# Optimization experiments

Measured on AMD Instinct MI355X. Metric: run time of the kernel, lower is better.

Reference implementation:

```python
import jax, jax.numpy as jnp
import numpy as np

N = 50000      # B*N nodes
K = 32         # top-k in-degree
E = N * K      # edges
IN_DIM = 128
EMB_DIM = 128
OUT_DIM = 128
HEADS = 4
D_HEAD = OUT_DIM // HEADS


def setup_inputs() -> dict:
    key = jax.random.key(0)
    ks = jax.random.split(key, 8)
    x = jax.random.normal(ks[0], (N, IN_DIM), dtype=jnp.float32)
    emb = jax.random.normal(ks[1], (N, EMB_DIM), dtype=jnp.float32)
    # top-k graph: each node i has exactly K in-neighbors (dst covers all nodes)
    dst = jnp.repeat(jnp.arange(N, dtype=jnp.int32), K)
    src = jax.random.randint(ks[2], (E,), 0, N, dtype=jnp.int32)
    edge_index = jnp.stack([src, dst], axis=0)
    # learned params (stored as (in, out); math-equivalent to torch Linear)
    W_q = jax.random.normal(ks[3], (EMB_DIM, OUT_DIM), dtype=jnp.float32) / np.sqrt(EMB_DIM)
    W_k = jax.random.normal(ks[4], (EMB_DIM, OUT_DIM), dtype=jnp.float32) / np.sqrt(EMB_DIM)
    W_v = jax.random.normal(ks[5], (IN_DIM + EMB_DIM, OUT_DIM), dtype=jnp.float32) / np.sqrt(IN_DIM + EMB_DIM)
    attn_vec = jax.random.normal(ks[6], (HEADS, 2 * D_HEAD), dtype=jnp.float32) / np.sqrt(2 * D_HEAD)
    ln_gamma = jnp.ones((OUT_DIM,), dtype=jnp.float32)
    ln_beta = jnp.zeros((OUT_DIM,), dtype=jnp.float32)
    return {"x": x, "emb": emb, "edge_index": edge_index, "W_q": W_q, "W_k": W_k,
            "W_v": W_v, "attn_vec": attn_vec, "ln_gamma": ln_gamma, "ln_beta": ln_beta}


def reference(x, emb, edge_index, W_q, W_k, W_v, attn_vec, ln_gamma, ln_beta):
    src, dst = edge_index[0], edge_index[1]
    BN = x.shape[0]
    H, D = HEADS, D_HEAD
    Q = (emb @ W_q).reshape(BN, H, D)
    K_ = (emb @ W_k).reshape(BN, H, D)
    # a^T [q_dst || k_src] = (a_q . q)_dst + (a_k . k)_src  (standard GAT split)
    a_q, a_k = attn_vec[:, :D], attn_vec[:, D:]
    sq = jnp.einsum('nhd,hd->nh', Q, a_q)   # (BN, H)
    sk = jnp.einsum('nhd,hd->nh', K_, a_k)  # (BN, H)
    e = sq[dst] + sk[src]                   # (E, H)
    e = jnp.where(e > 0, e, 0.2 * e)        # LeakyReLU(0.2)
    # segment softmax over incoming edges of each dst node
    e_max = jax.ops.segment_max(e, dst, num_segments=BN)
    e_exp = jnp.exp(e - e_max[dst])
    e_sum = jax.ops.segment_sum(e_exp, dst, num_segments=BN)
    alpha = e_exp / (e_sum[dst] + 1e-8)     # (E, H); dropout is identity at eval
    V = (jnp.concatenate([x, emb], axis=-1) @ W_v).reshape(BN, H, D)
    weighted = alpha[..., None] * V[src]    # (E, H, D)
    z = jax.ops.segment_sum(weighted, dst, num_segments=BN).reshape(BN, H * D)
    z = jax.nn.elu(z)
    mu = jnp.mean(z, axis=-1, keepdims=True)
    var = jnp.var(z, axis=-1, keepdims=True)
    return (z - mu) / jnp.sqrt(var + 1e-5) * ln_gamma + ln_beta
```

## Files before the change

kernel.cpp:

```cpp
#include <hip/hip_runtime.h>

#define NN 50000
#define KE 32
#define PAD_N 50048

using f32x4  = __attribute__((ext_vector_type(4))) float;
using bf16x8 = __attribute__((ext_vector_type(8))) short;

__device__ __forceinline__ ushort f2bf(float f) {
    union { float f; unsigned u; } c; c.f = f;
    unsigned u = c.u;
    u += 0x7fffu + ((u >> 16) & 1u);
    return (ushort)(u >> 16);
}

__global__ __launch_bounds__(256) void prep_kernel(const float* __restrict__ Wq,
        const float* __restrict__ Wk, const float* __restrict__ av,
        const float* __restrict__ Wv, ushort* __restrict__ Ub,
        ushort* __restrict__ Bt) {
    const int g = blockIdx.x * 256 + threadIdx.x;
    if (blockIdx.x < 2) {
        const int h = g >> 7, i = g & 127;
        float su = 0.f, sv = 0.f;
#pragma unroll
        for (int d = 0; d < 32; ++d) {
            su += Wq[i * 128 + h * 32 + d] * av[h * 64 + d];
            sv += Wk[i * 128 + h * 32 + d] * av[h * 64 + 32 + d];
        }
        Ub[h * 128 + i] = f2bf(su);
        Ub[(4 + h) * 128 + i] = f2bf(sv);
        Ub[1024 + g * 2] = 0;
        Ub[1024 + g * 2 + 1] = 0;
    } else {
        const int idx = g - 512;
        const int k = idx >> 7, n = idx & 127;
        Bt[n * 256 + k] = f2bf(Wv[idx]);
    }
}

__global__ __launch_bounds__(256) void vproj_mfma(const float* __restrict__ x,
        const float* __restrict__ emb, const ushort* __restrict__ Bt,
        const ushort* __restrict__ Ub, float* __restrict__ sqT,
        float* __restrict__ skT, ushort* __restrict__ Vp) {
    __shared__ short As[64 * 264];
    const int t = threadIdx.x;
    const int rbase = blockIdx.x * 64;
    const int wv = t >> 6;
    const int lane = t & 63;
    const int lo = lane & 15;
    const int quad = lane >> 4;
    const int c0 = wv * 32;

#pragma unroll
    for (int it = 0; it < 16; ++it) {
        const int li = it * 256 + t;
        const int row = li >> 6;
        const int c4 = li & 63;
        int rg = rbase + row; if (rg >= NN) rg = NN - 1;
        const float* sp = (c4 < 32) ? (x + (long)rg * 128 + c4 * 4)
                                    : (emb + (long)rg * 128 + (c4 - 32) * 4);
        float4 a = *(const float4*)sp;
        ushort4 b = make_ushort4(f2bf(a.x), f2bf(a.y), f2bf(a.z), f2bf(a.w));
        *(ushort4*)&As[row * 264 + c4 * 4] = b;
    }
    bf16x8 bt0[8], bt1[8];
#pragma unroll
    for (int ks = 0; ks < 8; ++ks) {
        const int kb = ks * 32 + quad * 8;
        bt0[ks] = *(const bf16x8*)(Bt + (c0 + lo) * 256 + kb);
        bt1[ks] = *(const bf16x8*)(Bt + (c0 + 16 + lo) * 256 + kb);
    }
    __syncthreads();

    f32x4 acc[4][2] = {};
#pragma unroll
    for (int ks = 0; ks < 8; ++ks) {
        const int kb = ks * 32 + quad * 8;
#pragma unroll
        for (int rt = 0; rt < 4; ++rt) {
            bf16x8 af = *(const bf16x8*)&As[(rt * 16 + lo) * 264 + kb];
            acc[rt][0] = __builtin_amdgcn_mfma_f32_16x16x32_bf16(af, bt0[ks], acc[rt][0], 0, 0, 0);
            acc[rt][1] = __builtin_amdgcn_mfma_f32_16x16x32_bf16(af, bt1[ks], acc[rt][1], 0, 0, 0);
        }
    }

    f32x4 sacc = {};
#pragma unroll
    for (int ks = 0; ks < 4; ++ks) {
        const int kk = ks * 32 + quad * 8;
        bf16x8 saf = *(const bf16x8*)&As[(wv * 16 + lo) * 264 + 128 + kk];
        bf16x8 sbf = *(const bf16x8*)(Ub + lo * 128 + kk);
        sacc = __builtin_amdgcn_mfma_f32_16x16x32_bf16(saf, sbf, sacc, 0, 0, 0);
    }
    if (lo < 8) {
#pragma unroll
        for (int r = 0; r < 4; ++r) {
            const int row = rbase + wv * 16 + quad * 4 + r;
            if (row < NN) {
                if (lo < 4) sqT[(long)lo * NN + row] = sacc[r];
                else        skT[(long)(lo - 4) * NN + row] = sacc[r];
            }
        }
    }

    __syncthreads();
#pragma unroll
    for (int rt = 0; rt < 4; ++rt)
#pragma unroll
        for (int ct = 0; ct < 2; ++ct)
#pragma unroll
            for (int r = 0; r < 4; ++r)
                As[(rt * 16 + quad * 4 + r) * 132 + c0 + ct * 16 + lo] =
                    (short)f2bf(acc[rt][ct][r]);
    __syncthreads();
#pragma unroll
    for (int i = 0; i < 4; ++i) {
        const int idx = i * 256 + t;
        const int row = idx >> 4;
        const int seg = idx & 15;
        const int grow = rbase + row;
        const int plane = seg >> 2;
        const int pc = (seg & 3) * 8;
        if (grow < NN)
            *(bf16x8*)(Vp + (long)plane * PAD_N * 32 + (long)grow * 32 + pc) =
                *(const bf16x8*)&As[row * 132 + seg * 8];
    }
}

__global__ __launch_bounds__(256) void gather_kernel(const int* __restrict__ src,
        const float* __restrict__ sqT, const float* __restrict__ skT,
        const ushort* __restrict__ Vp, float* __restrict__ z) {
    __shared__ int   s_src[64 * 33];
    __shared__ float s_al [64 * 33];
    const int b = blockIdx.x;
    const int head = (b & 7) >> 1;
    const int chunk = (b >> 3) * 2 + (b & 1);
    const int nbase = chunk * 64;
    const int t = threadIdx.x;
    const int e = t & 31;

    const float* sqh = sqT + (long)head * NN;
    const float* skh = skT + (long)head * NN;
#pragma unroll
    for (int p = 0; p < 8; ++p) {
        const int slot = p * 8 + (t >> 5);
        const int n = nbase + slot;
        const bool valid = n < NN;
        const int s = valid ? src[(long)n * KE + e] : 0;
        float ev = valid ? (sqh[n] + skh[s]) : 0.f;
        ev = ev > 0.f ? ev : 0.2f * ev;
        float m = ev;
#pragma unroll
        for (int off = 16; off > 0; off >>= 1)
            m = fmaxf(m, __shfl_xor(m, off));
        const float ex = __expf(ev - m);
        float sum = ex;
#pragma unroll
        for (int off = 16; off > 0; off >>= 1)
            sum += __shfl_xor(sum, off);
        s_src[slot * 33 + e] = s;
        s_al[slot * 33 + e] = ex / (sum + 1e-8f);
    }
    __syncthreads();

    const int slot = t >> 2;
    const int l = t & 3;
    const ushort* plane = Vp + (long)head * PAD_N * 32 + l * 8;
    float z0 = 0.f, z1 = 0.f, z2 = 0.f, z3 = 0.f;
    float z4 = 0.f, z5 = 0.f, z6 = 0.f, z7 = 0.f;
#pragma unroll 16
    for (int ee = 0; ee < 32; ++ee) {
        const int sidx = s_src[slot * 33 + ee];
        const float a = s_al[slot * 33 + ee];
        uint4 p = *(const uint4*)(plane + (long)sidx * 32);
        union { unsigned u; float f; } c0e, c0o, c1e, c1o, c2e, c2o, c3e, c3o;
        c0e.u = p.x << 16; c0o.u = p.x & 0xffff0000u;
        c1e.u = p.y << 16; c1o.u = p.y & 0xffff0000u;
        c2e.u = p.z << 16; c2o.u = p.z & 0xffff0000u;
        c3e.u = p.w << 16; c3o.u = p.w & 0xffff0000u;
        z0 += a * c0e.f; z1 += a * c0o.f;
        z2 += a * c1e.f; z3 += a * c1o.f;
        z4 += a * c2e.f; z5 += a * c2o.f;
        z6 += a * c3e.f; z7 += a * c3o.f;
    }
    const int node = nbase + slot;
    if (node < NN) {
        float* zp = z + (long)node * 128 + head * 32 + l * 8;
        *(float4*)(zp)     = make_float4(z0, z1, z2, z3);
        *(float4*)(zp + 4) = make_float4(z4, z5, z6, z7);
    }
}

__global__ __launch_bounds__(256) void lnorm_kernel(float* __restrict__ z,
        const float* __restrict__ gamma, const float* __restrict__ beta) {
    const int w = threadIdx.x >> 6;
    const int lane = threadIdx.x & 63;
    const int n = blockIdx.x * 4 + w;
    const int c0 = lane * 2;
    float2 zv = *(const float2*)(z + (long)n * 128 + c0);
    float zx = zv.x, zy = zv.y;
    zx = zx > 0.f ? zx : __expf(zx) - 1.f;
    zy = zy > 0.f ? zy : __expf(zy) - 1.f;
    float s1 = zx + zy;
    float s2 = zx * zx + zy * zy;
#pragma unroll
    for (int off = 32; off > 0; off >>= 1) {
        s1 += __shfl_xor(s1, off);
        s2 += __shfl_xor(s2, off);
    }
    const float mu = s1 * (1.f / 128.f);
    const float var = s2 * (1.f / 128.f) - mu * mu;
    const float rstd = rsqrtf(var + 1e-5f);
    float2 g = *(const float2*)(gamma + c0);
    float2 b = *(const float2*)(beta + c0);
    float2 o;
    o.x = (zx - mu) * rstd * g.x + b.x;
    o.y = (zy - mu) * rstd * g.y + b.y;
    *(float2*)(z + (long)n * 128 + c0) = o;
}

extern "C" void kernel_launch(void* const* d_in, const int* in_sizes, int n_in,
                              void* d_out, int out_size, void* d_ws, size_t ws_size,
                              hipStream_t stream) {
    const float* x     = (const float*)d_in[0];
    const float* emb   = (const float*)d_in[1];
    const int*   edge  = (const int*)d_in[2];
    const float* Wq    = (const float*)d_in[3];
    const float* Wk    = (const float*)d_in[4];
    const float* Wv    = (const float*)d_in[5];
    const float* av    = (const float*)d_in[6];
    const float* gamma = (const float*)d_in[7];
    const float* beta  = (const float*)d_in[8];
    float* out = (float*)d_out;

    char* ws = (char*)d_ws;
    ushort* Ub  = (ushort*)(ws + 0);
    ushort* Bt  = (ushort*)(ws + 4096);
    float*  sqT = (float*)(ws + 69632);
    float*  skT = (float*)(ws + 869632);
    ushort* Vp  = (ushort*)(ws + 1669632);

    prep_kernel<<<130, 256, 0, stream>>>(Wq, Wk, av, Wv, Ub, Bt);
    vproj_mfma<<<(NN + 63) / 64, 256, 0, stream>>>(x, emb, Bt, Ub, sqT, skT, Vp);
    gather_kernel<<<782 * 4, 256, 0, stream>>>(edge, sqT, skT, Vp, out);
    lnorm_kernel<<<NN / 4, 256, 0, stream>>>(out, gamma, beta);
}
```

Baseline: 195.7 us.

## Fuse per-head gather and layernorm into one all-heads aggregation kernel

Replaces the per-head gather kernel and separate layernorm kernel with one kernel that handles all four heads of a 64-node chunk. It computes the softmax for every head at once from node-major sq/sk float4 loads and reads the edge index list only once. ELU and layernorm are applied in registers before a single output write. This removes one kernel launch, the write and re-read of z, and the repeated src/score work per head. In exchange it uses more registers (32 indices plus a 4x8 accumulator), which lowers occupancy, and it stores alphas in fp16. The softmax also drops the max subtraction, so exp can overflow for large scores.

```diff
diff --git a/kernel.cpp b/kernel.cpp
--- a/kernel.cpp
+++ b/kernel.cpp
@@ -12,6 +12,12 @@
     unsigned u = c.u;
     u += 0x7fffu + ((u >> 16) & 1u);
     return (ushort)(u >> 16);
+}
+__device__ __forceinline__ ushort f2h(float f) {
+    union { _Float16 h; ushort u; } c; c.h = (_Float16)f; return c.u;
+}
+__device__ __forceinline__ float h2f(ushort u) {
+    union { ushort u; _Float16 h; } c; c.u = u; return (float)c.h;
 }
 
 __global__ __launch_bounds__(256) void prep_kernel(const float* __restrict__ Wq,
@@ -40,8 +46,8 @@
 
 __global__ __launch_bounds__(256) void vproj_mfma(const float* __restrict__ x,
         const float* __restrict__ emb, const ushort* __restrict__ Bt,
-        const ushort* __restrict__ Ub, float* __restrict__ sqT,
-        float* __restrict__ skT, ushort* __restrict__ Vp) {
+        const ushort* __restrict__ Ub, float* __restrict__ sq,
+        float* __restrict__ sk, ushort* __restrict__ Vp) {
     __shared__ short As[64 * 264];
     const int t = threadIdx.x;
     const int rbase = blockIdx.x * 64;
@@ -97,8 +103,8 @@
         for (int r = 0; r < 4; ++r) {
             const int row = rbase + wv * 16 + quad * 4 + r;
             if (row < NN) {
-                if (lo < 4) sqT[(long)lo * NN + row] = sacc[r];
-                else        skT[(long)(lo - 4) * NN + row] = sacc[r];
+                if (lo < 4) sq[(long)row * 4 + lo] = sacc[r];
+                else        sk[(long)row * 4 + lo - 4] = sacc[r];
             }
         }
     }
@@ -127,96 +133,118 @@
     }
 }
 
-__global__ __launch_bounds__(256) void gather_kernel(const int* __restrict__ src,
-        const float* __restrict__ sqT, const float* __restrict__ skT,
-        const ushort* __restrict__ Vp, float* __restrict__ z) {
-    __shared__ int   s_src[64 * 33];
-    __shared__ float s_al [64 * 33];
+__global__ __launch_bounds__(256) void aggregate2(const int* __restrict__ src,
+        const float* __restrict__ sq, const float* __restrict__ sk,
+        const ushort* __restrict__ Vp, const float* __restrict__ gamma,
+        const float* __restrict__ beta, float* __restrict__ out) {
+    __shared__ int    s_src[64 * 33];
+    __shared__ ushort s_al[4][64 * 33];
     const int b = blockIdx.x;
-    const int head = (b & 7) >> 1;
-    const int chunk = (b >> 3) * 2 + (b & 1);
-    const int nbase = chunk * 64;
+    const int nbase = b * 64;
     const int t = threadIdx.x;
     const int e = t & 31;
 
-    const float* sqh = sqT + (long)head * NN;
-    const float* skh = skT + (long)head * NN;
 #pragma unroll
     for (int p = 0; p < 8; ++p) {
         const int slot = p * 8 + (t >> 5);
         const int n = nbase + slot;
         const bool valid = n < NN;
         const int s = valid ? src[(long)n * KE + e] : 0;
-        float ev = valid ? (sqh[n] + skh[s]) : 0.f;
-        ev = ev > 0.f ? ev : 0.2f * ev;
-        float m = ev;
-#pragma unroll
-        for (int off = 16; off > 0; off >>= 1)
-            m = fmaxf(m, __shfl_xor(m, off));
-        const float ex = __expf(ev - m);
-        float sum = ex;
-#pragma unroll
-        for (int off = 16; off > 0; off >>= 1)
-            sum += __shfl_xor(sum, off);
+        float4 sk4 = *(const float4*)(sk + (long)s * 4);
+        float4 sq4 = *(const float4*)(sq + (long)(valid ? n : 0) * 4);
+        float ev[4] = { sq4.x + sk4.x, sq4.y + sk4.y, sq4.z + sk4.z, sq4.w + sk4.w };
+        float ex[4], sum[4];
+#pragma unroll
+        for (int h = 0; h < 4; ++h) {
+            float v = valid ? (ev[h] > 0.f ? ev[h] : 0.2f * ev[h]) : 0.f;
+            ex[h] = __expf(v);
+            sum[h] = ex[h];
+        }
+#pragma unroll
+        for (int off = 16; off > 0; off >>= 1) {
+#pragma unroll
+            for (int h = 0; h < 4; ++h) sum[h] += __shfl_xor(sum[h], off);
+        }
         s_src[slot * 33 + e] = s;
-        s_al[slot * 33 + e] = ex / (sum + 1e-8f);
+#pragma unroll
+        for (int h = 0; h < 4; ++h)
+            s_al[h][slot * 33 + e] = f2h(ex[h] / (sum[h] + 1e-8f));
     }
     __syncthreads();
 
     const int slot = t >> 2;
     const int l = t & 3;
-    const ushort* plane = Vp + (long)head * PAD_N * 32 + l * 8;
-    float z0 = 0.f, z1 = 0.f, z2 = 0.f, z3 = 0.f;
-    float z4 = 0.f, z5 = 0.f, z6 = 0.f, z7 = 0.f;
-#pragma unroll 16
-    for (int ee = 0; ee < 32; ++ee) {
-        const int sidx = s_src[slot * 33 + ee];
-        const float a = s_al[slot * 33 + ee];
-        uint4 p = *(const uint4*)(plane + (long)sidx * 32);
-        union { unsigned u; float f; } c0e, c0o, c1e, c1o, c2e, c2o, c3e, c3o;
-        c0e.u = p.x << 16; c0o.u = p.x & 0xffff0000u;
-        c1e.u = p.y << 16; c1o.u = p.y & 0xffff0000u;
-        c2e.u = p.z << 16; c2o.u = p.z & 0xffff0000u;
-        c3e.u = p.w << 16; c3o.u = p.w & 0xffff0000u;
-        z0 += a * c0e.f; z1 += a * c0o.f;
-        z2 += a * c1e.f; z3 += a * c1o.f;
-        z4 += a * c2e.f; z5 += a * c2o.f;
-        z6 += a * c3e.f; z7 += a * c3o.f;
-    }
     const int node = nbase + slot;
-    if (node < NN) {
-        float* zp = z + (long)node * 128 + head * 32 + l * 8;
-        *(float4*)(zp)     = make_float4(z0, z1, z2, z3);
-        *(float4*)(zp + 4) = make_float4(z4, z5, z6, z7);
-    }
-}
-
-__global__ __launch_bounds__(256) void lnorm_kernel(float* __restrict__ z,
-        const float* __restrict__ gamma, const float* __restrict__ beta) {
-    const int w = threadIdx.x >> 6;
-    const int lane = threadIdx.x & 63;
-    const int n = blockIdx.x * 4 + w;
-    const int c0 = lane * 2;
-    float2 zv = *(const float2*)(z + (long)n * 128 + c0);
-    float zx = zv.x, zy = zv.y;
-    zx = zx > 0.f ? zx : __expf(zx) - 1.f;
-    zy = zy > 0.f ? zy : __expf(zy) - 1.f;
-    float s1 = zx + zy;
-    float s2 = zx * zx + zy * zy;
-#pragma unroll
-    for (int off = 32; off > 0; off >>= 1) {
-        s1 += __shfl_xor(s1, off);
-        s2 += __shfl_xor(s2, off);
-    }
+    int sidx[32];
+#pragma unroll
+    for (int ee = 0; ee < 32; ++ee) sidx[ee] = s_src[slot * 33 + ee];
+
+    float z[4][8];
+    const int hstart = (b & 7) >> 1;
+#pragma unroll
+    for (int pp = 0; pp < 4; ++pp) {
+        const int h = (hstart + pp) & 3;
+        const ushort* plane = Vp + (long)h * PAD_N * 32 + l * 8;
+        const ushort* alh = &s_al[h][slot * 33];
+        float z0 = 0.f, z1 = 0.f, z2 = 0.f, z3 = 0.f;
+        float z4 = 0.f, z5 = 0.f, z6 = 0.f, z7 = 0.f;
+#pragma unroll
+        for (int ee = 0; ee < 32; ++ee) {
+            const float a = h2f(alh[ee]);
+            uint4 p = *(const uint4*)(plane + (long)sidx[ee] * 32);
+            union { unsigned u; float f; } c0e, c0o, c1e, c1o, c2e, c2o, c3e, c3o;
+            c0e.u = p.x << 16; c0o.u = p.x & 0xffff0000u;
+            c1e.u = p.y << 16; c1o.u = p.y & 0xffff0000u;
+            c2e.u = p.z << 16; c2o.u = p.z & 0xffff0000u;
+            c3e.u = p.w << 16; c3o.u = p.w & 0xffff0000u;
+            z0 += a * c0e.f; z1 += a * c0o.f;
+            z2 += a * c1e.f; z3 += a * c1o.f;
+            z4 += a * c2e.f; z5 += a * c2o.f;
+            z6 += a * c3e.f; z7 += a * c3o.f;
+        }
+        z[h][0] = z0; z[h][1] = z1; z[h][2] = z2; z[h][3] = z3;
+        z[h][4] = z4; z[h][5] = z5; z[h][6] = z6; z[h][7] = z7;
+        __syncthreads();
+    }
+
+    float s1 = 0.f, s2 = 0.f;
+#pragma unroll
+    for (int h = 0; h < 4; ++h)
+#pragma unroll
+        for (int j = 0; j < 8; ++j) {
+            float v = z[h][j];
+            v = v > 0.f ? v : __expf(v) - 1.f;
+            z[h][j] = v;
+            s1 += v;
+            s2 += v * v;
+        }
+    s1 += __shfl_xor(s1, 1); s1 += __shfl_xor(s1, 2);
+    s2 += __shfl_xor(s2, 1); s2 += __shfl_xor(s2, 2);
     const float mu = s1 * (1.f / 128.f);
     const float var = s2 * (1.f / 128.f) - mu * mu;
     const float rstd = rsqrtf(var + 1e-5f);
-    float2 g = *(const float2*)(gamma + c0);
-    float2 b = *(const float2*)(beta + c0);
-    float2 o;
-    o.x = (zx - mu) * rstd * g.x + b.x;
-    o.y = (zy - mu) * rstd * g.y + b.y;
-    *(float2*)(z + (long)n * 128 + c0) = o;
+    if (node < NN) {
+#pragma unroll
+        for (int h = 0; h < 4; ++h) {
+            const int c0 = h * 32 + l * 8;
+            float4 g0 = *(const float4*)(gamma + c0);
+            float4 g1 = *(const float4*)(gamma + c0 + 4);
+            float4 b0 = *(const float4*)(beta + c0);
+            float4 b1 = *(const float4*)(beta + c0 + 4);
+            float* zp = out + (long)node * 128 + c0;
+            float4 o0, o1;
+            o0.x = (z[h][0] - mu) * rstd * g0.x + b0.x;
+            o0.y = (z[h][1] - mu) * rstd * g0.y + b0.y;
+            o0.z = (z[h][2] - mu) * rstd * g0.z + b0.z;
+            o0.w = (z[h][3] - mu) * rstd * g0.w + b0.w;
+            o1.x = (z[h][4] - mu) * rstd * g1.x + b1.x;
+            o1.y = (z[h][5] - mu) * rstd * g1.y + b1.y;
+            o1.z = (z[h][6] - mu) * rstd * g1.z + b1.z;
+            o1.w = (z[h][7] - mu) * rstd * g1.w + b1.w;
+            *(float4*)(zp)     = o0;
+            *(float4*)(zp + 4) = o1;
+        }
+    }
 }
 
 extern "C" void kernel_launch(void* const* d_in, const int* in_sizes, int n_in,
@@ -234,14 +262,13 @@
     float* out = (float*)d_out;
 
     char* ws = (char*)d_ws;
-    ushort* Ub  = (ushort*)(ws + 0);
-    ushort* Bt  = (ushort*)(ws + 4096);
-    float*  sqT = (float*)(ws + 69632);
-    float*  skT = (float*)(ws + 869632);
-    ushort* Vp  = (ushort*)(ws + 1669632);
+    ushort* Ub = (ushort*)(ws + 0);
+    ushort* Bt = (ushort*)(ws + 4096);
+    float*  sq = (float*)(ws + 69632);
+    float*  sk = (float*)(ws + 869632);
+    ushort* Vp = (ushort*)(ws + 1669632);
 
     prep_kernel<<<130, 256, 0, stream>>>(Wq, Wk, av, Wv, Ub, Bt);
-    vproj_mfma<<<(NN + 63) / 64, 256, 0, stream>>>(x, emb, Bt, Ub, sqT, skT, Vp);
-    gather_kernel<<<782 * 4, 256, 0, stream>>>(edge, sqT, skT, Vp, out);
-    lnorm_kernel<<<NN / 4, 256, 0, stream>>>(out, gamma, beta);
-}
+    vproj_mfma<<<(NN + 63) / 64, 256, 0, stream>>>(x, emb, Bt, Ub, sq, sk, Vp);
+    aggregate2<<<(NN + 63) / 64, 256, 0, stream>>>(edge, sq, sk, Vp, gamma, beta, out);
+}
```

New measurement: 203.4 us. 1.04x slower.
